# Kernel tuning notes

Measured on AMD Instinct MI355X. Metric: run time of the kernel, lower is better.

## Reference

```python
import jax, jax.numpy as jnp
import numpy as np

N_NODES = 50000
N_EDGES = 600000
N_GRAPHS = 512
D = 128          # in_channels == hidden_channels
L = 4            # num_layers (total GINConv count)
N_CLASSES = 10
BN_EPS = 1e-5


def setup_inputs() -> dict:
    key = jax.random.key(0)
    ks = jax.random.split(key, 12)
    x = jax.random.normal(ks[0], (N_NODES, D), dtype=jnp.float32)
    edge_index = jax.random.randint(ks[1], (2, N_EDGES), 0, N_NODES, dtype=jnp.int64)
    batch = jnp.sort(jax.random.randint(ks[2], (N_NODES,), 0, N_GRAPHS, dtype=jnp.int64))
    s = 1.0 / np.sqrt(D)
    W1 = jax.random.uniform(ks[3], (L, D, D), jnp.float32, -s, s)
    b1 = jax.random.uniform(ks[4], (L, D), jnp.float32, -s, s)
    W2 = jax.random.uniform(ks[5], (L, D, D), jnp.float32, -s, s)
    b2 = jax.random.uniform(ks[6], (L, D), jnp.float32, -s, s)
    eps = jnp.zeros((L,), jnp.float32)            # train_eps=True, init 0
    gamma = jnp.ones((L, D), jnp.float32)
    beta = jnp.zeros((L, D), jnp.float32)
    sl = 1.0 / np.sqrt(D * L)
    Wlin = jax.random.uniform(ks[7], (D * L, N_CLASSES), jnp.float32, -sl, sl)
    blin = jax.random.uniform(ks[8], (N_CLASSES,), jnp.float32, -sl, sl)
    return {"x": x, "edge_index": edge_index, "batch": batch,
            "W1": W1, "b1": b1, "W2": W2, "b2": b2, "eps": eps,
            "gamma": gamma, "beta": beta, "Wlin": Wlin, "blin": blin}


def reference(x, edge_index, batch, W1, b1, W2, b2, eps, gamma, beta, Wlin, blin):
    src, dst = edge_index[0], edge_index[1]
    h = x
    pools = []
    for l in range(L):
        # GINConv: sum-aggregate neighbor features at dst, add (1+eps)*self
        agg = jax.ops.segment_sum(h[src], dst, num_segments=N_NODES)
        z = (1.0 + eps[l]) * h + agg
        # 2-layer MLP
        z = jnp.maximum(z @ W1[l] + b1[l], 0.0) @ W2[l] + b2[l]
        # BatchNorm1d (training mode: batch stats, biased variance)
        mean = jnp.mean(z, axis=0)
        var = jnp.mean(jnp.square(z - mean), axis=0)
        z = (z - mean) * jax.lax.rsqrt(var + BN_EPS) * gamma[l] + beta[l]
        h = jnp.maximum(z, 0.0)
        # global_add_pool per graph
        pools.append(jax.ops.segment_sum(h, batch, num_segments=N_GRAPHS))
    x_cat = jnp.concatenate(pools, axis=1)  # [N_GRAPHS, D*L]
    return x_cat @ Wlin + blin              # dropout = identity (eval)
```

## Files before the change

kernel.cpp:

```cpp
#include <hip/hip_runtime.h>

#define N_NODES 50000
#define N_EDGES 600000
#define N_GRAPHS 512
#define DIM 128
#define NLAYERS 4
#define NCLASSES 10
#define KPD 132

typedef __attribute__((ext_vector_type(8))) short short8;
typedef __attribute__((ext_vector_type(4))) float f32x4;

union Frag { short8 s; uint4 u; };

__device__ inline unsigned short f2bf(float v) {
    union { float f; unsigned u; } c; c.f = v;
    unsigned u = c.u;
    u += 0x7FFFu + ((u >> 16) & 1u);
    return (unsigned short)(u >> 16);
}
__device__ inline float bf2f(unsigned short h) {
    union { float f; unsigned u; } c; c.u = ((unsigned)h) << 16;
    return c.f;
}
__device__ inline float bfu_lo(unsigned u) {
    union { float f; unsigned x; } c; c.x = u << 16; return c.f;
}
__device__ inline float bfu_hi(unsigned u) {
    union { float f; unsigned x; } c; c.x = u & 0xFFFF0000u; return c.f;
}
__device__ inline void addRow(float* acc, const uint4& v) {
    acc[0] += bfu_lo(v.x); acc[1] += bfu_hi(v.x);
    acc[2] += bfu_lo(v.y); acc[3] += bfu_hi(v.y);
    acc[4] += bfu_lo(v.z); acc[5] += bfu_hi(v.z);
    acc[6] += bfu_lo(v.w); acc[7] += bfu_hi(v.w);
}

__global__ __launch_bounds__(256) void hist_kernel(
    const int* __restrict__ dst, int* __restrict__ deg)
{
    int e = blockIdx.x * 256 + threadIdx.x;
    if (e >= N_EDGES) return;
    atomicAdd(&deg[dst[e]], 1);
}

__global__ __launch_bounds__(256) void scan1_kernel(
    const int* __restrict__ deg, int* __restrict__ bsum)
{
    __shared__ int red[256];
    int t = threadIdx.x;
    int i4 = blockIdx.x * 256 + t;
    int s = 0;
    if (i4 < 12500) {
        int4 v = ((const int4*)deg)[i4];
        s = v.x + v.y + v.z + v.w;
    }
    red[t] = s;
    __syncthreads();
    for (int off = 128; off > 0; off >>= 1) {
        if (t < off) red[t] += red[t + off];
        __syncthreads();
    }
    if (t == 0) bsum[blockIdx.x] = red[0];
}

__global__ __launch_bounds__(64) void scan2_kernel(int* __restrict__ bsum)
{
    __shared__ int sh[64];
    int t = threadIdx.x;
    sh[t] = (t < 49) ? bsum[t] : 0;
    __syncthreads();
    if (t == 0) {
        int run = 0;
        for (int i = 0; i < 49; i++) { int v = sh[i]; sh[i] = run; run += v; }
    }
    __syncthreads();
    if (t < 49) bsum[t] = sh[t];
}

__global__ __launch_bounds__(256) void scan3_kernel(
    const int* __restrict__ deg, const int* __restrict__ bsum,
    int* __restrict__ rowptr, int* __restrict__ cursor)
{
    __shared__ int red[256];
    int t = threadIdx.x;
    int i4 = blockIdx.x * 256 + t;
    int4 v = {0, 0, 0, 0};
    if (i4 < 12500) v = ((const int4*)deg)[i4];
    int s = v.x + v.y + v.z + v.w;
    red[t] = s;
    __syncthreads();
    for (int off = 1; off < 256; off <<= 1) {
        int val = (t >= off) ? red[t - off] : 0;
        __syncthreads();
        red[t] += val;
        __syncthreads();
    }
    int run = bsum[blockIdx.x] + (t ? red[t - 1] : 0);
    if (i4 < 12500) {
        int4 rp;
        rp.x = run; run += v.x;
        rp.y = run; run += v.y;
        rp.z = run; run += v.z;
        rp.w = run; run += v.w;
        ((int4*)rowptr)[i4] = rp;
        ((int4*)cursor)[i4] = rp;
    }
    if (blockIdx.x == 0 && t == 0) rowptr[N_NODES] = N_EDGES;
}

__global__ __launch_bounds__(256) void fill_kernel(
    const int* __restrict__ src, const int* __restrict__ dst,
    int* __restrict__ cursor, int* __restrict__ csr)
{
    int e = blockIdx.x * 256 + threadIdx.x;
    if (e >= N_EDGES) return;
    int p = atomicAdd(&cursor[dst[e]], 1);
    csr[p] = src[e];
}

__global__ __launch_bounds__(256) void bounds_kernel(
    const int* __restrict__ batch, int* __restrict__ gstart)
{
    int n = blockIdx.x * 256 + threadIdx.x;
    if (n >= N_NODES) return;
    int b = batch[n];
    int bp = (n == 0) ? -1 : batch[n - 1];
    for (int g = bp + 1; g <= b; g++) gstart[g] = n;
    if (n == N_NODES - 1)
        for (int g = b + 1; g <= N_GRAPHS; g++) gstart[g] = N_NODES;
}

__global__ __launch_bounds__(256) void xconv_kernel(
    const float* __restrict__ x, unsigned int* __restrict__ xb)
{
    int idx = blockIdx.x * 256 + threadIdx.x;
    if (idx >= N_NODES * 32) return;
    float4 v = ((const float4*)x)[idx];
    uint2 o;
    o.x = (unsigned)f2bf(v.x) | ((unsigned)f2bf(v.y) << 16);
    o.y = (unsigned)f2bf(v.z) | ((unsigned)f2bf(v.w) << 16);
    ((uint2*)xb)[idx] = o;
}

__global__ __launch_bounds__(256) void wconv_kernel(
    const float* __restrict__ W1, const float* __restrict__ W2,
    unsigned short* __restrict__ whi)
{
    int idx = blockIdx.x * 256 + threadIdx.x;
    if (idx >= NLAYERS * 2 * 16384) return;
    int f   = idx & 16383;
    int w01 = (idx >> 14) & 1;
    int l   = idx >> 15;
    int j    = f & 7;
    int lane = (f >> 3) & 63;
    int cg   = (f >> 9) & 7;
    int ks   = f >> 12;
    int k = ks * 32 + (lane >> 4) * 8 + j;
    int n = cg * 16 + (lane & 15);
    const float* W = (w01 == 0 ? W1 : W2) + (size_t)l * 16384;
    whi[idx] = f2bf(W[k * 128 + n]);
}

__global__ __launch_bounds__(256) void gin_layer_kernel(
    const unsigned int* __restrict__ hb,
    const int* __restrict__ rowptr, const int* __restrict__ csr,
    const float* __restrict__ epsP,
    unsigned short* __restrict__ z,
    const unsigned short* __restrict__ whi,
    const float* __restrict__ b1, const float* __restrict__ b2,
    float* __restrict__ stats)
{
    __shared__ unsigned int tpk[64 * KPD];

    const int t = threadIdx.x;
    const int lane = t & 63;
    const int w = t >> 6;
    const int wr = w & 1, wc = w >> 1;
    const int l15 = lane & 15, quad = lane >> 4;
    const int base = blockIdx.x * 64;

    {
        const int m = t >> 2;
        const int c = t & 3;
        const int n = base + m;
        const uint4* hb4 = (const uint4*)hb;
        float acc[32];
        #pragma unroll
        for (int i = 0; i < 32; i++) acc[i] = 0.f;
        if (n < N_NODES) {
            const float e1 = 1.0f + epsP[0];
            const uint4* self = hb4 + (size_t)n * 16 + c * 4;
            #pragma unroll
            for (int j = 0; j < 4; j++) {
                uint4 v = self[j];
                float* a = acc + j * 8;
                a[0] = e1 * bfu_lo(v.x); a[1] = e1 * bfu_hi(v.x);
                a[2] = e1 * bfu_lo(v.y); a[3] = e1 * bfu_hi(v.y);
                a[4] = e1 * bfu_lo(v.z); a[5] = e1 * bfu_hi(v.z);
                a[6] = e1 * bfu_lo(v.w); a[7] = e1 * bfu_hi(v.w);
            }
            int beg = rowptr[n], end = rowptr[n + 1];
            int e = beg;
            if (e + 3 < end) {
                int s0 = csr[e], s1 = csr[e + 1], s2 = csr[e + 2], s3 = csr[e + 3];
                while (true) {
                    const uint4* r0 = hb4 + (size_t)s0 * 16 + c * 4;
                    const uint4* r1 = hb4 + (size_t)s1 * 16 + c * 4;
                    const uint4* r2 = hb4 + (size_t)s2 * 16 + c * 4;
                    const uint4* r3 = hb4 + (size_t)s3 * 16 + c * 4;
                    uint4 v00 = r0[0], v01 = r0[1], v02 = r0[2], v03 = r0[3];
                    uint4 v10 = r1[0], v11 = r1[1], v12 = r1[2], v13 = r1[3];
                    uint4 v20 = r2[0], v21 = r2[1], v22 = r2[2], v23 = r2[3];
                    uint4 v30 = r3[0], v31 = r3[1], v32 = r3[2], v33 = r3[3];
                    int en = e + 4;
                    bool more = (en + 3 < end);
                    if (more) {
                        s0 = csr[en]; s1 = csr[en + 1];
                        s2 = csr[en + 2]; s3 = csr[en + 3];
                    }
                    addRow(acc + 0, v00); addRow(acc + 8, v01); addRow(acc + 16, v02); addRow(acc + 24, v03);
                    addRow(acc + 0, v10); addRow(acc + 8, v11); addRow(acc + 16, v12); addRow(acc + 24, v13);
                    addRow(acc + 0, v20); addRow(acc + 8, v21); addRow(acc + 16, v22); addRow(acc + 24, v23);
                    addRow(acc + 0, v30); addRow(acc + 8, v31); addRow(acc + 16, v32); addRow(acc + 24, v33);
                    e = en;
                    if (!more) break;
                }
            }
            for (; e < end; e++) {
                int s0 = csr[e];
                const uint4* r0 = hb4 + (size_t)s0 * 16 + c * 4;
                uint4 a0 = r0[0], a1 = r0[1], a2 = r0[2], a3 = r0[3];
                addRow(acc + 0, a0);  addRow(acc + 8, a1);
                addRow(acc + 16, a2); addRow(acc + 24, a3);
            }
        }
        uint4* dp = (uint4*)&tpk[m * KPD + c * 32];
        #pragma unroll
        for (int v4 = 0; v4 < 8; v4++) {
            uint4 pk;
            unsigned* pp = (unsigned*)&pk;
            #pragma unroll
            for (int j = 0; j < 4; j++) {
                float vv = acc[v4 * 4 + j];
                unsigned short h = f2bf(vv);
                unsigned short lo = f2bf(vv - bf2f(h));
                pp[j] = (unsigned)h | ((unsigned)lo << 16);
            }
            dp[v4] = pk;
        }
    }
    __syncthreads();

    f32x4 acc[2][4];
    #pragma unroll
    for (int s = 0; s < 2; s++)
        #pragma unroll
        for (int i = 0; i < 4; i++) acc[s][i] = (f32x4){0.f, 0.f, 0.f, 0.f};

    const int arowd0 = (32 * wr + l15) * KPD;
    const int arowd1 = arowd0 + 16 * KPD;

    #pragma unroll
    for (int kh = 0; kh < 2; kh++) {
        Frag bf[2][4];
        uint4 u00[2], u01[2], u10[2], u11[2];
        #pragma unroll
        for (int kk = 0; kk < 2; kk++) {
            int ks = kh * 2 + kk;
            #pragma unroll
            for (int i = 0; i < 4; i++) {
                size_t woff = (size_t)(((ks * 8 + wc * 4 + i) * 64 + lane) * 8);
                bf[kk][i].s = *((const short8*)&whi[woff]);
            }
            int kd = ks * 32 + quad * 8;
            u00[kk] = *((uint4*)&tpk[arowd0 + kd]);
            u01[kk] = *((uint4*)&tpk[arowd0 + kd + 4]);
            u10[kk] = *((uint4*)&tpk[arowd1 + kd]);
            u11[kk] = *((uint4*)&tpk[arowd1 + kd + 4]);
        }
        #pragma unroll
        for (int kk = 0; kk < 2; kk++) {
            Frag ah0, al0, ah1, al1;
            ah0.u = (uint4){ (u00[kk].x & 0xFFFFu) | (u00[kk].y << 16),
                             (u00[kk].z & 0xFFFFu) | (u00[kk].w << 16),
                             (u01[kk].x & 0xFFFFu) | (u01[kk].y << 16),
                             (u01[kk].z & 0xFFFFu) | (u01[kk].w << 16) };
            al0.u = (uint4){ (u00[kk].x >> 16) | (u00[kk].y & 0xFFFF0000u),
                             (u00[kk].z >> 16) | (u00[kk].w & 0xFFFF0000u),
                             (u01[kk].x >> 16) | (u01[kk].y & 0xFFFF0000u),
                             (u01[kk].z >> 16) | (u01[kk].w & 0xFFFF0000u) };
            ah1.u = (uint4){ (u10[kk].x & 0xFFFFu) | (u10[kk].y << 16),
                             (u10[kk].z & 0xFFFFu) | (u10[kk].w << 16),
                             (u11[kk].x & 0xFFFFu) | (u11[kk].y << 16),
                             (u11[kk].z & 0xFFFFu) | (u11[kk].w << 16) };
            al1.u = (uint4){ (u10[kk].x >> 16) | (u10[kk].y & 0xFFFF0000u),
                             (u10[kk].z >> 16) | (u10[kk].w & 0xFFFF0000u),
                             (u11[kk].x >> 16) | (u11[kk].y & 0xFFFF0000u),
                             (u11[kk].z >> 16) | (u11[kk].w & 0xFFFF0000u) };
            #pragma unroll
            for (int i = 0; i < 4; i++) {
                acc[0][i] = __builtin_amdgcn_mfma_f32_16x16x32_bf16(al0.s, bf[kk][i].s, acc[0][i], 0, 0, 0);
                acc[0][i] = __builtin_amdgcn_mfma_f32_16x16x32_bf16(ah0.s, bf[kk][i].s, acc[0][i], 0, 0, 0);
                acc[1][i] = __builtin_amdgcn_mfma_f32_16x16x32_bf16(al1.s, bf[kk][i].s, acc[1][i], 0, 0, 0);
                acc[1][i] = __builtin_amdgcn_mfma_f32_16x16x32_bf16(ah1.s, bf[kk][i].s, acc[1][i], 0, 0, 0);
            }
        }
    }
    __syncthreads();

    #pragma unroll
    for (int i = 0; i < 4; i++) {
        int col = wc * 64 + i * 16 + l15;
        float bb = b1[col];
        #pragma unroll
        for (int s = 0; s < 2; s++) {
            #pragma unroll
            for (int r = 0; r < 4; r++) {
                int m = 32 * wr + 16 * s + quad * 4 + r;
                float v = fmaxf(acc[s][i][r] + bb, 0.f);
                unsigned short h = f2bf(v);
                unsigned short lo2 = f2bf(v - bf2f(h));
                tpk[m * KPD + col] = (unsigned)h | ((unsigned)lo2 << 16);
            }
            acc[s][i] = (f32x4){0.f, 0.f, 0.f, 0.f};
        }
    }
    __syncthreads();

    const unsigned short* w2 = whi + 16384;
    #pragma unroll
    for (int kh = 0; kh < 2; kh++) {
        Frag bf[2][4];
        uint4 u00[2], u01[2], u10[2], u11[2];
        #pragma unroll
        for (int kk = 0; kk < 2; kk++) {
            int ks = kh * 2 + kk;
            #pragma unroll
            for (int i = 0; i < 4; i++) {
                size_t woff = (size_t)(((ks * 8 + wc * 4 + i) * 64 + lane) * 8);
                bf[kk][i].s = *((const short8*)&w2[woff]);
            }
            int kd = ks * 32 + quad * 8;
            u00[kk] = *((uint4*)&tpk[arowd0 + kd]);
            u01[kk] = *((uint4*)&tpk[arowd0 + kd + 4]);
            u10[kk] = *((uint4*)&tpk[arowd1 + kd]);
            u11[kk] = *((uint4*)&tpk[arowd1 + kd + 4]);
        }
        #pragma unroll
        for (int kk = 0; kk < 2; kk++) {
            Frag ah0, al0, ah1, al1;
            ah0.u = (uint4){ (u00[kk].x & 0xFFFFu) | (u00[kk].y << 16),
                             (u00[kk].z & 0xFFFFu) | (u00[kk].w << 16),
                             (u01[kk].x & 0xFFFFu) | (u01[kk].y << 16),
                             (u01[kk].z & 0xFFFFu) | (u01[kk].w << 16) };
            al0.u = (uint4){ (u00[kk].x >> 16) | (u00[kk].y & 0xFFFF0000u),
                             (u00[kk].z >> 16) | (u00[kk].w & 0xFFFF0000u),
                             (u01[kk].x >> 16) | (u01[kk].y & 0xFFFF0000u),
                             (u01[kk].z >> 16) | (u01[kk].w & 0xFFFF0000u) };
            ah1.u = (uint4){ (u10[kk].x & 0xFFFFu) | (u10[kk].y << 16),
                             (u10[kk].z & 0xFFFFu) | (u10[kk].w << 16),
                             (u11[kk].x & 0xFFFFu) | (u11[kk].y << 16),
                             (u11[kk].z & 0xFFFFu) | (u11[kk].w << 16) };
            al1.u = (uint4){ (u10[kk].x >> 16) | (u10[kk].y & 0xFFFF0000u),
                             (u10[kk].z >> 16) | (u10[kk].w & 0xFFFF0000u),
                             (u11[kk].x >> 16) | (u11[kk].y & 0xFFFF0000u),
                             (u11[kk].z >> 16) | (u11[kk].w & 0xFFFF0000u) };
            #pragma unroll
            for (int i = 0; i < 4; i++) {
                acc[0][i] = __builtin_amdgcn_mfma_f32_16x16x32_bf16(al0.s, bf[kk][i].s, acc[0][i], 0, 0, 0);
                acc[0][i] = __builtin_amdgcn_mfma_f32_16x16x32_bf16(ah0.s, bf[kk][i].s, acc[0][i], 0, 0, 0);
                acc[1][i] = __builtin_amdgcn_mfma_f32_16x16x32_bf16(al1.s, bf[kk][i].s, acc[1][i], 0, 0, 0);
                acc[1][i] = __builtin_amdgcn_mfma_f32_16x16x32_bf16(ah1.s, bf[kk][i].s, acc[1][i], 0, 0, 0);
            }
        }
    }
    __syncthreads();

    unsigned short* zs = (unsigned short*)tpk;
    float* sums = (float*)((char*)tpk + 20480);
    float* sqs  = sums + 1024;
    {
        float colsum[4], colsq[4];
        #pragma unroll
        for (int i = 0; i < 4; i++) {
            int col = wc * 64 + i * 16 + l15;
            float bb = b2[col];
            float su = 0.f, q2 = 0.f;
            #pragma unroll
            for (int s = 0; s < 2; s++) {
                #pragma unroll
                for (int r = 0; r < 4; r++) {
                    int m = 32 * wr + 16 * s + quad * 4 + r;
                    int n = base + m;
                    float v = acc[s][i][r] + bb;
                    zs[m * 136 + col] = f2bf(v);
                    if (n < N_NODES) { su += v; q2 += v * v; }
                }
            }
            colsum[i] = su; colsq[i] = q2;
        }
        #pragma unroll
        for (int i = 0; i < 4; i++) {
            sums[(w * 4 + i) * 64 + lane] = colsum[i];
            sqs [(w * 4 + i) * 64 + lane] = colsq[i];
        }
    }
    __syncthreads();

    {
        int m2 = t >> 2, c2 = t & 3;
        int n2 = base + m2;
        if (n2 < N_NODES) {
            const uint4* srcp = (const uint4*)(zs + m2 * 136 + c2 * 32);
            uint4* dstp = (uint4*)z + (size_t)n2 * 16 + c2 * 4;
            #pragma unroll
            for (int j = 0; j < 4; j++) dstp[j] = srcp[j];
        }
    }
    if (t < 128) {
        int c = t;
        int wcc = c >> 6, ci = (c >> 4) & 3, cl = c & 15;
        float s = 0.f, q2 = 0.f;
        #pragma unroll
        for (int wrr = 0; wrr < 2; wrr++) {
            int ww = wcc * 2 + wrr;
            #pragma unroll
            for (int u = 0; u < 4; u++) {
                int ln = cl + u * 16;
                s  += sums[(ww * 4 + ci) * 64 + ln];
                q2 += sqs [(ww * 4 + ci) * 64 + ln];
            }
        }
        unsafeAtomicAdd(&stats[c], s);
        unsafeAtomicAdd(&stats[128 + c], q2);
    }
}

__global__ __launch_bounds__(256) void bnpool_kernel(
    const unsigned int* __restrict__ z, const float* __restrict__ stats,
    const float* __restrict__ gamma, const float* __restrict__ beta,
    const int* __restrict__ gstart, unsigned int* __restrict__ hout,
    float* __restrict__ pools, int layer)
{
    __shared__ float red[8][128];
    const int g = blockIdx.x;
    const int t = threadIdx.x;
    const int q = t & 31, r = t >> 5;
    const int beg = gstart[g], end = gstart[g + 1];

    float4 s  = ((const float4*)stats)[q];
    float4 sq = ((const float4*)stats)[32 + q];
    float4 gm = ((const float4*)gamma)[q];
    float4 bt = ((const float4*)beta)[q];
    const float invN = 1.0f / (float)N_NODES;
    float m, vr;
    float4 scl, sh;
    m = s.x * invN; vr = sq.x * invN - m * m; scl.x = gm.x * rsqrtf(vr + 1e-5f); sh.x = bt.x - m * scl.x;
    m = s.y * invN; vr = sq.y * invN - m * m; scl.y = gm.y * rsqrtf(vr + 1e-5f); sh.y = bt.y - m * scl.y;
    m = s.z * invN; vr = sq.z * invN - m * m; scl.z = gm.z * rsqrtf(vr + 1e-5f); sh.z = bt.z - m * scl.z;
    m = s.w * invN; vr = sq.w * invN - m * m; scl.w = gm.w * rsqrtf(vr + 1e-5f); sh.w = bt.w - m * scl.w;

    float4 acc = {0.f, 0.f, 0.f, 0.f};
    for (int n = beg + r; n < end; n += 8) {
        uint2 zp = ((const uint2*)z)[(size_t)n * 32 + q];
        float4 hv;
        hv.x = fmaxf(bfu_lo(zp.x) * scl.x + sh.x, 0.f);
        hv.y = fmaxf(bfu_hi(zp.x) * scl.y + sh.y, 0.f);
        hv.z = fmaxf(bfu_lo(zp.y) * scl.z + sh.z, 0.f);
        hv.w = fmaxf(bfu_hi(zp.y) * scl.w + sh.w, 0.f);
        uint2 p;
        p.x = (unsigned)f2bf(hv.x) | ((unsigned)f2bf(hv.y) << 16);
        p.y = (unsigned)f2bf(hv.z) | ((unsigned)f2bf(hv.w) << 16);
        ((uint2*)hout)[(size_t)n * 32 + q] = p;
        acc.x += hv.x; acc.y += hv.y; acc.z += hv.z; acc.w += hv.w;
    }
    red[r][q * 4 + 0] = acc.x;
    red[r][q * 4 + 1] = acc.y;
    red[r][q * 4 + 2] = acc.z;
    red[r][q * 4 + 3] = acc.w;
    __syncthreads();
    if (t < 128) {
        float sm = 0.f;
        #pragma unroll
        for (int rr = 0; rr < 8; rr++) sm += red[rr][t];
        pools[(size_t)g * (DIM * NLAYERS) + (size_t)layer * DIM + t] = sm;
    }
}

__global__ __launch_bounds__(64) void final_kernel(
    const float* __restrict__ pools, const float* __restrict__ Wlin,
    const float* __restrict__ blin, float* __restrict__ out)
{
    int g = blockIdx.x;
    int lane = threadIdx.x;
    const float* xr = pools + (size_t)g * (DIM * NLAYERS);
    float a[NCLASSES];
    #pragma unroll
    for (int o = 0; o < NCLASSES; o++) a[o] = 0.f;
    for (int kk = 0; kk < DIM * NLAYERS; kk += 64) {
        float xv = xr[kk + lane];
        const float* wr = Wlin + (size_t)(kk + lane) * NCLASSES;
        #pragma unroll
        for (int o = 0; o < NCLASSES; o++) a[o] += xv * wr[o];
    }
    #pragma unroll
    for (int o = 0; o < NCLASSES; o++) {
        float v = a[o];
        #pragma unroll
        for (int off = 32; off > 0; off >>= 1) v += __shfl_down(v, off, 64);
        if (lane == 0) out[(size_t)g * NCLASSES + o] = v + blin[o];
    }
}

extern "C" void kernel_launch(void* const* d_in, const int* in_sizes, int n_in,
                              void* d_out, int out_size, void* d_ws, size_t ws_size,
                              hipStream_t stream)
{
    const float* x     = (const float*)d_in[0];
    const int*   src   = (const int*)d_in[1];
    const int*   dst   = ((const int*)d_in[1]) + N_EDGES;
    const int*   batch = (const int*)d_in[2];
    const float* W1    = (const float*)d_in[3];
    const float* b1    = (const float*)d_in[4];
    const float* W2    = (const float*)d_in[5];
    const float* b2    = (const float*)d_in[6];
    const float* eps   = (const float*)d_in[7];
    const float* gamma = (const float*)d_in[8];
    const float* beta  = (const float*)d_in[9];
    const float* Wlin  = (const float*)d_in[10];
    const float* blin  = (const float*)d_in[11];
    float* out = (float*)d_out;

    char* ws = (char*)d_ws;
    const size_t FEATH = (size_t)N_NODES * DIM * sizeof(unsigned short);
    size_t off = 0;
    unsigned int* buf_h = (unsigned int*)(ws + off); off += FEATH;
    unsigned short* buf_z = (unsigned short*)(ws + off); off += FEATH;
    float* pools  = (float*)(ws + off); off += (size_t)N_GRAPHS * DIM * NLAYERS * sizeof(float);
    float* stats  = (float*)(ws + off); off += (size_t)NLAYERS * 256 * sizeof(float);
    int*   deg    = (int*)(ws + off);   off += (size_t)N_NODES * sizeof(int);
    int*   rowptr = (int*)(ws + off);   off += (size_t)(N_NODES + 1) * sizeof(int) + 12;
    int*   csr    = (int*)(ws + off);   off += (size_t)N_EDGES * sizeof(int);
    int*   gstart = (int*)(ws + off);   off += 2064;
    int*   bsum   = (int*)(ws + off);   off += 208;
    unsigned short* whi = (unsigned short*)(ws + off); off += (size_t)NLAYERS * 2 * 16384 * 2;

    hipMemsetAsync(stats, 0, (size_t)NLAYERS * 256 * sizeof(float), stream);
    hipMemsetAsync(deg, 0, (size_t)N_NODES * sizeof(int), stream);

    hist_kernel<<<(N_EDGES + 255) / 256, 256, 0, stream>>>(dst, deg);
    scan1_kernel<<<49, 256, 0, stream>>>(deg, bsum);
    scan2_kernel<<<1, 64, 0, stream>>>(bsum);
    scan3_kernel<<<49, 256, 0, stream>>>(deg, bsum, rowptr, deg );
    fill_kernel<<<(N_EDGES + 255) / 256, 256, 0, stream>>>(src, dst, deg, csr);
    bounds_kernel<<<(N_NODES + 255) / 256, 256, 0, stream>>>(batch, gstart);
    xconv_kernel<<<(N_NODES * 32 + 255) / 256, 256, 0, stream>>>(x, buf_h);
    wconv_kernel<<<(NLAYERS * 2 * 16384 + 255) / 256, 256, 0, stream>>>(W1, W2, whi);

    for (int l = 0; l < NLAYERS; l++) {
        gin_layer_kernel<<<(N_NODES + 63) / 64, 256, 0, stream>>>(
            buf_h, rowptr, csr, eps + l, buf_z,
            whi + (size_t)l * 32768,
            b1 + (size_t)l * DIM, b2 + (size_t)l * DIM,
            stats + (size_t)l * 256);
        bnpool_kernel<<<N_GRAPHS, 256, 0, stream>>>(
            (const unsigned int*)buf_z, stats + (size_t)l * 256,
            gamma + (size_t)l * DIM, beta + (size_t)l * DIM,
            gstart, buf_h, pools, l);
    }
    final_kernel<<<N_GRAPHS, 64, 0, stream>>>(pools, Wlin, blin, out);
}
```

Measured before the change: 415.8 us.

## Drop split-bf16 hi/lo MFMA emulation and interleave gather column chunks

Aggregated features and hidden activations were stored as packed hi/lo bf16 pairs and multiplied with two MFMAs per tile to approximate fp32 precision. They are now stored as a single bf16 value, which halves MFMA work and LDS footprint and removes the unpacking ALU work. The neighbour gather also changes so the four threads of a row read interleaved 16-byte chunks, which makes each load instruction coalesced across threads. The cost is lower precision in the MLP inputs, which may affect accuracy tolerance.

```diff
diff --git a/kernel.cpp b/kernel.cpp
--- a/kernel.cpp
+++ b/kernel.cpp
@@ -6,7 +6,7 @@
 #define DIM 128
 #define NLAYERS 4
 #define NCLASSES 10
-#define KPD 132
+#define KPS 136
 
 typedef __attribute__((ext_vector_type(8))) short short8;
 typedef __attribute__((ext_vector_type(4))) float f32x4;
@@ -18,10 +18,6 @@
     unsigned u = c.u;
     u += 0x7FFFu + ((u >> 16) & 1u);
     return (unsigned short)(u >> 16);
-}
-__device__ inline float bf2f(unsigned short h) {
-    union { float f; unsigned u; } c; c.u = ((unsigned)h) << 16;
-    return c.f;
 }
 __device__ inline float bfu_lo(unsigned u) {
     union { float f; unsigned x; } c; c.x = u << 16; return c.f;
@@ -171,7 +167,9 @@
     const float* __restrict__ b1, const float* __restrict__ b2,
     float* __restrict__ stats)
 {
-    __shared__ unsigned int tpk[64 * KPD];
+    __shared__ unsigned short tpk[64 * KPS];
+    __shared__ float sums[1024];
+    __shared__ float sqs[1024];
 
     const int t = threadIdx.x;
     const int lane = t & 63;
@@ -190,10 +188,10 @@
         for (int i = 0; i < 32; i++) acc[i] = 0.f;
         if (n < N_NODES) {
             const float e1 = 1.0f + epsP[0];
-            const uint4* self = hb4 + (size_t)n * 16 + c * 4;
+            const uint4* self = hb4 + (size_t)n * 16 + c;
             #pragma unroll
             for (int j = 0; j < 4; j++) {
-                uint4 v = self[j];
+                uint4 v = self[j * 4];
                 float* a = acc + j * 8;
                 a[0] = e1 * bfu_lo(v.x); a[1] = e1 * bfu_hi(v.x);
                 a[2] = e1 * bfu_lo(v.y); a[3] = e1 * bfu_hi(v.y);
@@ -205,14 +203,14 @@
             if (e + 3 < end) {
                 int s0 = csr[e], s1 = csr[e + 1], s2 = csr[e + 2], s3 = csr[e + 3];
                 while (true) {
-                    const uint4* r0 = hb4 + (size_t)s0 * 16 + c * 4;
-                    const uint4* r1 = hb4 + (size_t)s1 * 16 + c * 4;
-                    const uint4* r2 = hb4 + (size_t)s2 * 16 + c * 4;
-                    const uint4* r3 = hb4 + (size_t)s3 * 16 + c * 4;
-                    uint4 v00 = r0[0], v01 = r0[1], v02 = r0[2], v03 = r0[3];
-                    uint4 v10 = r1[0], v11 = r1[1], v12 = r1[2], v13 = r1[3];
-                    uint4 v20 = r2[0], v21 = r2[1], v22 = r2[2], v23 = r2[3];
-                    uint4 v30 = r3[0], v31 = r3[1], v32 = r3[2], v33 = r3[3];
+                    const uint4* r0 = hb4 + (size_t)s0 * 16 + c;
+                    const uint4* r1 = hb4 + (size_t)s1 * 16 + c;
+                    const uint4* r2 = hb4 + (size_t)s2 * 16 + c;
+                    const uint4* r3 = hb4 + (size_t)s3 * 16 + c;
+                    uint4 v00 = r0[0], v01 = r0[4], v02 = r0[8], v03 = r0[12];
+                    uint4 v10 = r1[0], v11 = r1[4], v12 = r1[8], v13 = r1[12];
+                    uint4 v20 = r2[0], v21 = r2[4], v22 = r2[8], v23 = r2[12];
+                    uint4 v30 = r3[0], v31 = r3[4], v32 = r3[8], v33 = r3[12];
                     int en = e + 4;
                     bool more = (en + 3 < end);
                     if (more) {
@@ -229,25 +227,18 @@
             }
             for (; e < end; e++) {
                 int s0 = csr[e];
-                const uint4* r0 = hb4 + (size_t)s0 * 16 + c * 4;
-                uint4 a0 = r0[0], a1 = r0[1], a2 = r0[2], a3 = r0[3];
+                const uint4* r0 = hb4 + (size_t)s0 * 16 + c;
+                uint4 a0 = r0[0], a1 = r0[4], a2 = r0[8], a3 = r0[12];
                 addRow(acc + 0, a0);  addRow(acc + 8, a1);
                 addRow(acc + 16, a2); addRow(acc + 24, a3);
             }
         }
-        uint4* dp = (uint4*)&tpk[m * KPD + c * 32];
-        #pragma unroll
-        for (int v4 = 0; v4 < 8; v4++) {
-            uint4 pk;
-            unsigned* pp = (unsigned*)&pk;
-            #pragma unroll
-            for (int j = 0; j < 4; j++) {
-                float vv = acc[v4 * 4 + j];
-                unsigned short h = f2bf(vv);
-                unsigned short lo = f2bf(vv - bf2f(h));
-                pp[j] = (unsigned)h | ((unsigned)lo << 16);
-            }
-            dp[v4] = pk;
+        #pragma unroll
+        for (int j = 0; j < 4; j++) {
+            union { short8 s; unsigned short u[8]; } pk;
+            #pragma unroll
+            for (int i = 0; i < 8; i++) pk.u[i] = f2bf(acc[j * 8 + i]);
+            *((short8*)&tpk[m * KPS + j * 32 + c * 8]) = pk.s;
         }
     }
     __syncthreads();
@@ -258,13 +249,13 @@
         #pragma unroll
         for (int i = 0; i < 4; i++) acc[s][i] = (f32x4){0.f, 0.f, 0.f, 0.f};
 
-    const int arowd0 = (32 * wr + l15) * KPD;
-    const int arowd1 = arowd0 + 16 * KPD;
+    const int arow0 = (32 * wr + l15) * KPS;
+    const int arow1 = arow0 + 16 * KPS;
 
     #pragma unroll
     for (int kh = 0; kh < 2; kh++) {
         Frag bf[2][4];
-        uint4 u00[2], u01[2], u10[2], u11[2];
+        short8 a0[2], a1[2];
         #pragma unroll
         for (int kk = 0; kk < 2; kk++) {
             int ks = kh * 2 + kk;
@@ -273,37 +264,15 @@
                 size_t woff = (size_t)(((ks * 8 + wc * 4 + i) * 64 + lane) * 8);
                 bf[kk][i].s = *((const short8*)&whi[woff]);
             }
-            int kd = ks * 32 + quad * 8;
-            u00[kk] = *((uint4*)&tpk[arowd0 + kd]);
-            u01[kk] = *((uint4*)&tpk[arowd0 + kd + 4]);
-            u10[kk] = *((uint4*)&tpk[arowd1 + kd]);
-            u11[kk] = *((uint4*)&tpk[arowd1 + kd + 4]);
+            a0[kk] = *((const short8*)&tpk[arow0 + ks * 32 + quad * 8]);
+            a1[kk] = *((const short8*)&tpk[arow1 + ks * 32 + quad * 8]);
         }
         #pragma unroll
         for (int kk = 0; kk < 2; kk++) {
-            Frag ah0, al0, ah1, al1;
-            ah0.u = (uint4){ (u00[kk].x & 0xFFFFu) | (u00[kk].y << 16),
-                             (u00[kk].z & 0xFFFFu) | (u00[kk].w << 16),
-                             (u01[kk].x & 0xFFFFu) | (u01[kk].y << 16),
-                             (u01[kk].z & 0xFFFFu) | (u01[kk].w << 16) };
-            al0.u = (uint4){ (u00[kk].x >> 16) | (u00[kk].y & 0xFFFF0000u),
-                             (u00[kk].z >> 16) | (u00[kk].w & 0xFFFF0000u),
-                             (u01[kk].x >> 16) | (u01[kk].y & 0xFFFF0000u),
-                             (u01[kk].z >> 16) | (u01[kk].w & 0xFFFF0000u) };
-            ah1.u = (uint4){ (u10[kk].x & 0xFFFFu) | (u10[kk].y << 16),
-                             (u10[kk].z & 0xFFFFu) | (u10[kk].w << 16),
-                             (u11[kk].x & 0xFFFFu) | (u11[kk].y << 16),
-                             (u11[kk].z & 0xFFFFu) | (u11[kk].w << 16) };
-            al1.u = (uint4){ (u10[kk].x >> 16) | (u10[kk].y & 0xFFFF0000u),
-                             (u10[kk].z >> 16) | (u10[kk].w & 0xFFFF0000u),
-                             (u11[kk].x >> 16) | (u11[kk].y & 0xFFFF0000u),
-                             (u11[kk].z >> 16) | (u11[kk].w & 0xFFFF0000u) };
             #pragma unroll
             for (int i = 0; i < 4; i++) {
-                acc[0][i] = __builtin_amdgcn_mfma_f32_16x16x32_bf16(al0.s, bf[kk][i].s, acc[0][i], 0, 0, 0);
-                acc[0][i] = __builtin_amdgcn_mfma_f32_16x16x32_bf16(ah0.s, bf[kk][i].s, acc[0][i], 0, 0, 0);
-                acc[1][i] = __builtin_amdgcn_mfma_f32_16x16x32_bf16(al1.s, bf[kk][i].s, acc[1][i], 0, 0, 0);
-                acc[1][i] = __builtin_amdgcn_mfma_f32_16x16x32_bf16(ah1.s, bf[kk][i].s, acc[1][i], 0, 0, 0);
+                acc[0][i] = __builtin_amdgcn_mfma_f32_16x16x32_bf16(a0[kk], bf[kk][i].s, acc[0][i], 0, 0, 0);
+                acc[1][i] = __builtin_amdgcn_mfma_f32_16x16x32_bf16(a1[kk], bf[kk][i].s, acc[1][i], 0, 0, 0);
             }
         }
     }
@@ -319,9 +288,7 @@
             for (int r = 0; r < 4; r++) {
                 int m = 32 * wr + 16 * s + quad * 4 + r;
                 float v = fmaxf(acc[s][i][r] + bb, 0.f);
-                unsigned short h = f2bf(v);
-                unsigned short lo2 = f2bf(v - bf2f(h));
-                tpk[m * KPD + col] = (unsigned)h | ((unsigned)lo2 << 16);
+                tpk[m * KPS + col] = f2bf(v);
             }
             acc[s][i] = (f32x4){0.f, 0.f, 0.f, 0.f};
         }
@@ -332,7 +299,7 @@
     #pragma unroll
     for (int kh = 0; kh < 2; kh++) {
         Frag bf[2][4];
-        uint4 u00[2], u01[2], u10[2], u11[2];
+        short8 a0[2], a1[2];
         #pragma unroll
         for (int kk = 0; kk < 2; kk++) {
             int ks = kh * 2 + kk;
@@ -341,45 +308,20 @@
                 size_t woff = (size_t)(((ks * 8 + wc * 4 + i) * 64 + lane) * 8);
                 bf[kk][i].s = *((const short8*)&w2[woff]);
             }
-            int kd = ks * 32 + quad * 8;
-            u00[kk] = *((uint4*)&tpk[arowd0 + kd]);
-            u01[kk] = *((uint4*)&tpk[arowd0 + kd + 4]);
-            u10[kk] = *((uint4*)&tpk[arowd1 + kd]);
-            u11[kk] = *((uint4*)&tpk[arowd1 + kd + 4]);
+            a0[kk] = *((const short8*)&tpk[arow0 + ks * 32 + quad * 8]);
+            a1[kk] = *((const short8*)&tpk[arow1 + ks * 32 + quad * 8]);
         }
         #pragma unroll
         for (int kk = 0; kk < 2; kk++) {
-            Frag ah0, al0, ah1, al1;
-            ah0.u = (uint4){ (u00[kk].x & 0xFFFFu) | (u00[kk].y << 16),
-                             (u00[kk].z & 0xFFFFu) | (u00[kk].w << 16),
-                             (u01[kk].x & 0xFFFFu) | (u01[kk].y << 16),
-                             (u01[kk].z & 0xFFFFu) | (u01[kk].w << 16) };
-            al0.u = (uint4){ (u00[kk].x >> 16) | (u00[kk].y & 0xFFFF0000u),
-                             (u00[kk].z >> 16) | (u00[kk].w & 0xFFFF0000u),
-                             (u01[kk].x >> 16) | (u01[kk].y & 0xFFFF0000u),
-                             (u01[kk].z >> 16) | (u01[kk].w & 0xFFFF0000u) };
-            ah1.u = (uint4){ (u10[kk].x & 0xFFFFu) | (u10[kk].y << 16),
-                             (u10[kk].z & 0xFFFFu) | (u10[kk].w << 16),
-                             (u11[kk].x & 0xFFFFu) | (u11[kk].y << 16),
-                             (u11[kk].z & 0xFFFFu) | (u11[kk].w << 16) };
-            al1.u = (uint4){ (u10[kk].x >> 16) | (u10[kk].y & 0xFFFF0000u),
-                             (u10[kk].z >> 16) | (u10[kk].w & 0xFFFF0000u),
-                             (u11[kk].x >> 16) | (u11[kk].y & 0xFFFF0000u),
-                             (u11[kk].z >> 16) | (u11[kk].w & 0xFFFF0000u) };
             #pragma unroll
             for (int i = 0; i < 4; i++) {
-                acc[0][i] = __builtin_amdgcn_mfma_f32_16x16x32_bf16(al0.s, bf[kk][i].s, acc[0][i], 0, 0, 0);
-                acc[0][i] = __builtin_amdgcn_mfma_f32_16x16x32_bf16(ah0.s, bf[kk][i].s, acc[0][i], 0, 0, 0);
-                acc[1][i] = __builtin_amdgcn_mfma_f32_16x16x32_bf16(al1.s, bf[kk][i].s, acc[1][i], 0, 0, 0);
-                acc[1][i] = __builtin_amdgcn_mfma_f32_16x16x32_bf16(ah1.s, bf[kk][i].s, acc[1][i], 0, 0, 0);
-            }
-        }
-    }
-    __syncthreads();
-
-    unsigned short* zs = (unsigned short*)tpk;
-    float* sums = (float*)((char*)tpk + 20480);
-    float* sqs  = sums + 1024;
+                acc[0][i] = __builtin_amdgcn_mfma_f32_16x16x32_bf16(a0[kk], bf[kk][i].s, acc[0][i], 0, 0, 0);
+                acc[1][i] = __builtin_amdgcn_mfma_f32_16x16x32_bf16(a1[kk], bf[kk][i].s, acc[1][i], 0, 0, 0);
+            }
+        }
+    }
+    __syncthreads();
+
     {
         float colsum[4], colsq[4];
         #pragma unroll
@@ -394,7 +336,7 @@
                     int m = 32 * wr + 16 * s + quad * 4 + r;
                     int n = base + m;
                     float v = acc[s][i][r] + bb;
-                    zs[m * 136 + col] = f2bf(v);
+                    tpk[m * KPS + col] = f2bf(v);
                     if (n < N_NODES) { su += v; q2 += v * v; }
                 }
             }
@@ -412,10 +354,10 @@
         int m2 = t >> 2, c2 = t & 3;
         int n2 = base + m2;
         if (n2 < N_NODES) {
-            const uint4* srcp = (const uint4*)(zs + m2 * 136 + c2 * 32);
-            uint4* dstp = (uint4*)z + (size_t)n2 * 16 + c2 * 4;
-            #pragma unroll
-            for (int j = 0; j < 4; j++) dstp[j] = srcp[j];
+            const uint4* srcp = (const uint4*)(tpk + m2 * KPS);
+            uint4* dstp = (uint4*)z + (size_t)n2 * 16;
+            #pragma unroll
+            for (int j = 0; j < 4; j++) dstp[j * 4 + c2] = srcp[j * 4 + c2];
         }
     }
     if (t < 128) {
```

Measured after the change: 410.1 us. No clear change (-1.4%).
